# Kernel optimization log

Measured on AMD Instinct MI355X. Metric: run time of the kernel, lower is better.

The kernel has to match this reference:

```python
import jax, jax.numpy as jnp
import numpy as np

N = 100_000   # nodes
E = 1_600_000 # edges
D = 128       # input feature dim
H = 128       # hidden dim


def _lin_params(key, fan_in, fan_out):
    # torch nn.Linear default init: U(-1/sqrt(fan_in), 1/sqrt(fan_in))
    kw, kb = jax.random.split(key)
    s = 1.0 / np.sqrt(fan_in)
    W = jax.random.uniform(kw, (fan_in, fan_out), jnp.float32, -s, s)
    b = jax.random.uniform(kb, (fan_out,), jnp.float32, -s, s)
    return W, b


def setup_inputs() -> dict:
    key = jax.random.key(0)
    ks = jax.random.split(key, 9)
    x = jax.random.normal(ks[0], (N, D), jnp.float32)
    edge_index = jax.random.randint(ks[1], (2, E), 0, N)
    W1, b1 = _lin_params(ks[2], D, H)   # GCN layer 1
    W2, b2 = _lin_params(ks[3], H, H)   # GCN layer 2
    W3, b3 = _lin_params(ks[4], H, H)   # GCN layer 3
    sW1, sb1 = _lin_params(ks[5], 2 * H, 2 * H)  # scorer MLP
    sW2, sb2 = _lin_params(ks[6], 2 * H, H)
    sW3, sb3 = _lin_params(ks[7], H, 1)
    return {"x": x, "edge_index": edge_index,
            "W1": W1, "b1": b1, "W2": W2, "b2": b2, "W3": W3, "b3": b3,
            "sW1": sW1, "sb1": sb1, "sW2": sW2, "sb2": sb2, "sW3": sW3, "sb3": sb3}


def gcn_conv(h, src, tgt, W, b, n_nodes):
    # PyG GCNConv: add self-loops, D^{-1/2}(A+I)D^{-1/2} X W + b
    h = h @ W  # [N, out]
    deg = jax.ops.segment_sum(jnp.ones(src.shape[0], h.dtype), tgt,
                              num_segments=n_nodes) + 1.0  # +1 for self-loop
    dis = jax.lax.rsqrt(deg)                               # deg>=1 so finite
    coef = dis[src] * dis[tgt]                             # [E]
    agg = jax.ops.segment_sum(h[src] * coef[:, None], tgt, num_segments=n_nodes)
    agg = agg + h * (dis * dis)[:, None]                   # self-loop messages
    return agg + b


def reference(x, edge_index, W1, b1, W2, b2, W3, b3, sW1, sb1, sW2, sb2, sW3, sb3):
    src, tgt = edge_index[0], edge_index[1]
    n = x.shape[0]
    h = x
    for W, b in ((W1, b1), (W2, b2), (W3, b3)):
        h = jax.nn.relu(gcn_conv(h, src, tgt, W, b, n))
    node_embs = jnp.nan_to_num(h, nan=0.0)
    # edge scorer: gather src/tgt embeddings, concat, 3-layer MLP
    edge_feat = jnp.concatenate([node_embs[src], node_embs[tgt]], axis=1)  # [E, 2H]
    z = jax.nn.relu(edge_feat @ sW1 + sb1)
    z = jax.nn.relu(z @ sW2 + sb2)
    score = (z @ sW3 + sb3)[:, 0]  # [E]
    score = jnp.clip(score, -1e6, 1e6)
    score = jnp.nan_to_num(score, nan=0.0, posinf=1e6, neginf=-1e6)
    return score, node_embs
```

## Files before the change

kernel.cpp:

```cpp
#include <hip/hip_runtime.h>
#include <hip/hip_bf16.h>


#define SCORER_G 4

typedef __attribute__((ext_vector_type(8))) short bf16x8;
typedef __attribute__((ext_vector_type(4))) float f32x4;

__device__ __forceinline__ unsigned short f2bf(float x) {
  unsigned u = __float_as_uint(x);
  return (unsigned short)((u + 0x7FFFu + ((u >> 16) & 1u)) >> 16);
}
__device__ __forceinline__ float bf2f(unsigned short b) {
  return __uint_as_float(((unsigned)b) << 16);
}


__global__ __launch_bounds__(256) void zero_i32(int* __restrict__ p, int n) {
  int i = blockIdx.x * 256 + threadIdx.x;
  if (i < n) p[i] = 0;
}

__global__ __launch_bounds__(256) void deg_count(const int* __restrict__ tgt,
                                                 int* __restrict__ deg, int E) {
  int e = blockIdx.x * 256 + threadIdx.x;
  if (e < E) atomicAdd(&deg[tgt[e]], 1);
}

__global__ __launch_bounds__(256) void scan1(const int* __restrict__ deg,
                                             int* __restrict__ rowptr,
                                             int* __restrict__ bsum, int N) {
  __shared__ int s[256];
  int tid = threadIdx.x;
  int i = blockIdx.x * 256 + tid;
  int v = (i < N) ? deg[i] : 0;
  s[tid] = v;
  __syncthreads();
  for (int off = 1; off < 256; off <<= 1) {
    int t = (tid >= off) ? s[tid - off] : 0;
    __syncthreads();
    s[tid] += t;
    __syncthreads();
  }
  if (i < N) rowptr[i + 1] = s[tid];
  if (tid == 255) bsum[blockIdx.x] = s[255];
}

__global__ __launch_bounds__(512) void scan2(int* __restrict__ bsum, int nb) {
  __shared__ int s[512];
  int tid = threadIdx.x;
  int v = (tid < nb) ? bsum[tid] : 0;
  s[tid] = v;
  __syncthreads();
  for (int off = 1; off < 512; off <<= 1) {
    int t = (tid >= off) ? s[tid - off] : 0;
    __syncthreads();
    s[tid] += t;
    __syncthreads();
  }
  if (tid < nb) bsum[tid] = s[tid] - v;
}

__global__ __launch_bounds__(256) void scan3(int* __restrict__ rowptr,
                                             int* __restrict__ cursor,
                                             const int* __restrict__ bsum,
                                             float* __restrict__ dis, int N) {
  int i = blockIdx.x * 256 + threadIdx.x;
  if (i >= N) return;
  int incl = rowptr[i + 1] + bsum[blockIdx.x];
  rowptr[i + 1] = incl;
  int d = cursor[i];
  cursor[i] = incl - d;
  dis[i] = rsqrtf((float)d + 1.0f);
  if (i == 0) rowptr[0] = 0;
}

__global__ __launch_bounds__(256) void fill_k(const int* __restrict__ tgt,
                                              int* __restrict__ cursor,
                                              int* __restrict__ csr_eid, int E) {
  int e = blockIdx.x * 256 + threadIdx.x;
  if (e >= E) return;
  int pos = atomicAdd(&cursor[tgt[e]], 1);
  csr_eid[pos] = e;
}

__global__ __launch_bounds__(256) void wsplit_k(const float* __restrict__ sW2,
                                                unsigned short* __restrict__ Wth,
                                                unsigned short* __restrict__ Wtl) {
  int id = blockIdx.x * 256 + threadIdx.x;
  if (id >= 128 * 256) return;
  int n = id >> 8, k = id & 255;
  float v = sW2[k * 128 + n];
  unsigned short h = f2bf(v);
  Wth[id] = h;
  Wtl[id] = f2bf(v - bf2f(h));
}

__global__ __launch_bounds__(256) void gemm_k(const float* __restrict__ A,
                                              const float* __restrict__ W,
                                              float* __restrict__ out,
                                              int nRows, int nout) {
  __shared__ float As[64][36];
  __shared__ float Ws[32][128];
  const int tid  = threadIdx.x;
  const int row0 = blockIdx.x * 64;
  const int col0 = blockIdx.y * 128;
  const bool full = (row0 + 64 <= nRows);
  const int ty = tid >> 5, tx = tid & 31;
  const int r0 = ty * 8, c0 = tx * 4;
  float acc[8][4] = {};
  for (int kt = 0; kt < 128; kt += 32) {
    if (full) {
#pragma unroll
      for (int j = 0; j < 2; ++j) {
        int chunk = tid + j * 256;
        int r = chunk >> 3, c4 = (chunk & 7) * 4;
        *(float4*)(&As[r][c4]) =
            *(const float4*)(A + (size_t)(row0 + r) * 128 + kt + c4);
      }
    } else {
#pragma unroll
      for (int j = 0; j < 2; ++j) {
        int chunk = tid + j * 256;
        int r = chunk >> 3, c4 = (chunk & 7) * 4;
        float4 v = make_float4(0.f, 0.f, 0.f, 0.f);
        int gr = row0 + r;
        if (gr < nRows) v = *(const float4*)(A + (size_t)gr * 128 + kt + c4);
        *(float4*)(&As[r][c4]) = v;
      }
    }
#pragma unroll
    for (int j = 0; j < 4; ++j) {
      int chunk = tid + j * 256;
      int wr = chunk >> 5, wc4 = (chunk & 31) * 4;
      *(float4*)(&Ws[wr][wc4]) =
          *(const float4*)(W + (size_t)(kt + wr) * nout + col0 + wc4);
    }
    __syncthreads();
#pragma unroll
    for (int kk = 0; kk < 8; ++kk) {
      const float4 wv0 = *(const float4*)(&Ws[kk * 4 + 0][c0]);
      const float4 wv1 = *(const float4*)(&Ws[kk * 4 + 1][c0]);
      const float4 wv2 = *(const float4*)(&Ws[kk * 4 + 2][c0]);
      const float4 wv3 = *(const float4*)(&Ws[kk * 4 + 3][c0]);
#pragma unroll
      for (int i = 0; i < 8; ++i) {
        const float4 av = *(const float4*)(&As[r0 + i][kk * 4]);
        acc[i][0] += av.x * wv0.x + av.y * wv1.x + av.z * wv2.x + av.w * wv3.x;
        acc[i][1] += av.x * wv0.y + av.y * wv1.y + av.z * wv2.y + av.w * wv3.y;
        acc[i][2] += av.x * wv0.z + av.y * wv1.z + av.z * wv2.z + av.w * wv3.z;
        acc[i][3] += av.x * wv0.w + av.y * wv1.w + av.z * wv2.w + av.w * wv3.w;
      }
    }
    __syncthreads();
  }
#pragma unroll
  for (int i = 0; i < 8; ++i) {
    int gr = row0 + r0 + i;
    if (gr < nRows) {
      float4 v = make_float4(acc[i][0], acc[i][1], acc[i][2], acc[i][3]);
      *(float4*)(out + (size_t)gr * nout + col0 + c0) = v;
    }
  }
}

__global__ __launch_bounds__(256) void agg_k(const int* __restrict__ rowptr,
                                             const int* __restrict__ csr_eid,
                                             const int* __restrict__ src0,
                                             const float* __restrict__ dis,
                                             const float* __restrict__ hw,
                                             const float* __restrict__ bias,
                                             float* __restrict__ out, int N) {
  int i = (blockIdx.x * 256 + threadIdx.x) >> 6;
  if (i >= N) return;
  int l = threadIdx.x & 63;
  const float di = dis[i];
  const float2 bb = *(const float2*)(bias + l * 2);
  float2 acc = *(const float2*)(hw + (size_t)i * 128 + l * 2);
  float sc = di * di;
  acc.x *= sc; acc.y *= sc;
  int e = rowptr[i], e1 = rowptr[i + 1];
  for (; e + 1 < e1; e += 2) {
    int eA = csr_eid[e], eB = csr_eid[e + 1];
    int sA = src0[eA], sB = src0[eB];
    float cA = dis[sA] * di, cB = dis[sB] * di;
    const float2 vA = *(const float2*)(hw + (size_t)sA * 128 + l * 2);
    const float2 vB = *(const float2*)(hw + (size_t)sB * 128 + l * 2);
    acc.x += vA.x * cA + vB.x * cB;
    acc.y += vA.y * cA + vB.y * cB;
  }
  if (e < e1) {
    int eA = csr_eid[e];
    int sA = src0[eA];
    float cA = dis[sA] * di;
    const float2 vA = *(const float2*)(hw + (size_t)sA * 128 + l * 2);
    acc.x += vA.x * cA;
    acc.y += vA.y * cA;
  }
  acc.x = fmaxf(acc.x + bb.x, 0.f);
  acc.y = fmaxf(acc.y + bb.y, 0.f);
  *(float2*)(out + (size_t)i * 128 + l * 2) = acc;
}

__global__ __launch_bounds__(512, 4) void scorer_k(
    const float* __restrict__ Amat, const float* __restrict__ Bmat,
    const int* __restrict__ csr_eid, const int* __restrict__ src0,
    const int* __restrict__ tgt0, const float* __restrict__ sb1,
    const unsigned short* __restrict__ Wth,
    const unsigned short* __restrict__ Wtl,
    const float* __restrict__ sb2, const float* __restrict__ sW3,
    const float* __restrict__ sb3, float* __restrict__ score, int E) {
  __shared__ unsigned short z1h[64][256];
  __shared__ unsigned short z1l[64][256];
  __shared__ float psum[2][64];
  const int tid  = threadIdx.x;
  const int lane = tid & 63;
  const int wv   = tid >> 6;
  const int mb   = wv & 3;
  const int half = wv >> 2;
  const int l15  = lane & 15;
  const int l4   = lane >> 4;
  const float4 bb  = *(const float4*)(sb1 + lane * 4);
  const float sb3s = sb3[0];
  float sb2q[4], w3q[4];
#pragma unroll
  for (int q = 0; q < 4; ++q) {
    int col = (half * 4 + q) * 16 + l15;
    sb2q[q] = sb2[col];
    w3q[q]  = sW3[col];
  }
  char* z1h_b = (char*)&z1h[0][0];
  char* z1l_b = (char*)&z1l[0][0];

  for (int g = 0; g < SCORER_G; ++g) {
    const int e0 = (blockIdx.x * SCORER_G + g) * 64;
    if (e0 >= E) break;

#pragma unroll
    for (int j = 0; j < 8; ++j) {
      int row = wv * 8 + j;
      int e = e0 + row;
      if (e >= E) e = E - 1;
      int eid = csr_eid[e];
      int s = src0[eid], t = tgt0[eid];
      float4 a = *(const float4*)(Amat + (size_t)s * 256 + lane * 4);
      float4 b = *(const float4*)(Bmat + (size_t)t * 256 + lane * 4);
      float z0 = fmaxf(a.x + b.x + bb.x, 0.f);
      float z1v = fmaxf(a.y + b.y + bb.y, 0.f);
      float z2v = fmaxf(a.z + b.z + bb.z, 0.f);
      float z3v = fmaxf(a.w + b.w + bb.w, 0.f);
      ushort4 hp, lp;
      hp.x = f2bf(z0);  lp.x = f2bf(z0 - bf2f(hp.x));
      hp.y = f2bf(z1v); lp.y = f2bf(z1v - bf2f(hp.y));
      hp.z = f2bf(z2v); lp.z = f2bf(z2v - bf2f(hp.z));
      hp.w = f2bf(z3v); lp.w = f2bf(z3v - bf2f(hp.w));
      int bofs = (row * 512 + lane * 8) ^ ((row & 7) << 4);
      *(ushort4*)(z1h_b + bofs) = hp;
      *(ushort4*)(z1l_b + bofs) = lp;
    }
    __syncthreads();

    f32x4 acc0 = {0.f, 0.f, 0.f, 0.f};
    f32x4 acc1 = acc0, acc2 = acc0, acc3 = acc0;
    const int arow = mb * 16 + l15;
    const int aswz = (arow & 7) << 4;
#pragma unroll
    for (int kts = 0; kts < 8; ++kts) {
      int abofs = (arow * 512 + kts * 64 + l4 * 16) ^ aswz;
      bf16x8 ah = *(const bf16x8*)(z1h_b + abofs);
      bf16x8 al = *(const bf16x8*)(z1l_b + abofs);
      const int kof = kts * 32 + l4 * 8;
#define BQ(q)                                                                 \
      {                                                                       \
        int n = (half * 4 + (q)) * 16 + l15;                                  \
        bf16x8 bh = *(const bf16x8*)(Wth + n * 256 + kof);                    \
        bf16x8 bl = *(const bf16x8*)(Wtl + n * 256 + kof);                    \
        acc##q = __builtin_amdgcn_mfma_f32_16x16x32_bf16(al, bh, acc##q, 0, 0, 0); \
        acc##q = __builtin_amdgcn_mfma_f32_16x16x32_bf16(ah, bl, acc##q, 0, 0, 0); \
        acc##q = __builtin_amdgcn_mfma_f32_16x16x32_bf16(ah, bh, acc##q, 0, 0, 0); \
      }
      BQ(0) BQ(1) BQ(2) BQ(3)
#undef BQ
    }

    float t0 = 0.f, t1 = 0.f, t2 = 0.f, t3 = 0.f;
#define EQ(q)                                                   \
    t0 += fmaxf(acc##q[0] + sb2q[q], 0.f) * w3q[q];             \
    t1 += fmaxf(acc##q[1] + sb2q[q], 0.f) * w3q[q];             \
    t2 += fmaxf(acc##q[2] + sb2q[q], 0.f) * w3q[q];             \
    t3 += fmaxf(acc##q[3] + sb2q[q], 0.f) * w3q[q];
    EQ(0) EQ(1) EQ(2) EQ(3)
#undef EQ
#pragma unroll
    for (int m = 8; m >= 1; m >>= 1) {
      t0 += __shfl_xor(t0, m, 64);
      t1 += __shfl_xor(t1, m, 64);
      t2 += __shfl_xor(t2, m, 64);
      t3 += __shfl_xor(t3, m, 64);
    }
    if (l15 == 0) {
      int rb = mb * 16 + l4 * 4;
      psum[half][rb + 0] = t0;
      psum[half][rb + 1] = t1;
      psum[half][rb + 2] = t2;
      psum[half][rb + 3] = t3;
    }
    __syncthreads();
    if (tid < 64) {
      float v = psum[0][tid] + psum[1][tid] + sb3s;
      v = fminf(fmaxf(v, -1e6f), 1e6f);
      if (v != v) v = 0.f;
      int e = e0 + tid;
      if (e < E) score[csr_eid[e]] = v;
    }
    __syncthreads();
  }
}


extern "C" void kernel_launch(void* const* d_in, const int* in_sizes, int n_in,
                              void* d_out, int out_size, void* d_ws, size_t ws_size,
                              hipStream_t stream) {
  const float* x   = (const float*)d_in[0];
  const int*   ei  = (const int*)d_in[1];
  const float* W1  = (const float*)d_in[2];
  const float* b1  = (const float*)d_in[3];
  const float* W2  = (const float*)d_in[4];
  const float* b2  = (const float*)d_in[5];
  const float* W3  = (const float*)d_in[6];
  const float* b3  = (const float*)d_in[7];
  const float* sW1 = (const float*)d_in[8];
  const float* sb1 = (const float*)d_in[9];
  const float* sW2 = (const float*)d_in[10];
  const float* sb2 = (const float*)d_in[11];
  const float* sW3 = (const float*)d_in[12];
  const float* sb3 = (const float*)d_in[13];

  const int N = in_sizes[0] / 128;
  const int E = in_sizes[1] / 2;
  const int* src0 = ei;
  const int* tgt0 = ei + E;

  float* out_score = (float*)d_out;
  float* out_emb   = out_score + E;

  float* ws = (float*)d_ws;
  float* dis     = ws;
  int*   rowptr  = (int*)(dis + N);
  int*   csr_eid = rowptr + (N + 4);
  float* Abuf    = (float*)(csr_eid + E);
  float* Bbuf    = Abuf + (size_t)N * 256;
  unsigned short* Wth = (unsigned short*)(Bbuf + (size_t)N * 256);
  unsigned short* Wtl = Wth + 128 * 256;
  int*   cursor  = (int*)Abuf;
  int*   bsum    = cursor + N;
  float* hw      = Abuf;

  const dim3 blk(256);
  const int gN  = (N + 255) / 256;
  const int gE  = (E + 255) / 256;
  const int gRows = (N + 63) / 64;
  const int gAgg  = (N * 64 + 255) / 256;
  const int nT64  = (E + 63) / 64;
  const int gScore = (nT64 + SCORER_G - 1) / SCORER_G;

  zero_i32<<<gN, blk, 0, stream>>>(cursor, N);
  deg_count<<<gE, blk, 0, stream>>>(tgt0, cursor, E);
  scan1<<<gN, blk, 0, stream>>>(cursor, rowptr, bsum, N);
  scan2<<<1, 512, 0, stream>>>(bsum, gN);
  scan3<<<gN, blk, 0, stream>>>(rowptr, cursor, bsum, dis, N);
  fill_k<<<gE, blk, 0, stream>>>(tgt0, cursor, csr_eid, E);

  wsplit_k<<<128, blk, 0, stream>>>(sW2, Wth, Wtl);

  gemm_k<<<dim3(gRows, 1), blk, 0, stream>>>(x, W1, hw, N, 128);
  agg_k<<<gAgg, blk, 0, stream>>>(rowptr, csr_eid, src0, dis, hw, b1, out_emb, N);
  gemm_k<<<dim3(gRows, 1), blk, 0, stream>>>(out_emb, W2, hw, N, 128);
  agg_k<<<gAgg, blk, 0, stream>>>(rowptr, csr_eid, src0, dis, hw, b2, out_emb, N);
  gemm_k<<<dim3(gRows, 1), blk, 0, stream>>>(out_emb, W3, hw, N, 128);
  agg_k<<<gAgg, blk, 0, stream>>>(rowptr, csr_eid, src0, dis, hw, b3, out_emb, N);

  gemm_k<<<dim3(gRows, 2), blk, 0, stream>>>(out_emb, sW1, Abuf, N, 256);
  gemm_k<<<dim3(gRows, 2), blk, 0, stream>>>(out_emb, sW1 + 128 * 256, Bbuf, N, 256);

  scorer_k<<<gScore, dim3(512), 0, stream>>>(Abuf, Bbuf, csr_eid, src0, tgt0,
                                             sb1, Wth, Wtl, sb2, sW3, sb3,
                                             out_score, E);
}
```

Measured before the change: 3.087 ms.

## Keep scorer W2 tiles in registers and split waves by output column

```diff
diff --git a/kernel.cpp b/kernel.cpp
--- a/kernel.cpp
+++ b/kernel.cpp
@@ -212,102 +212,116 @@
     const float* __restrict__ sb3, float* __restrict__ score, int E) {
   __shared__ unsigned short z1h[64][256];
   __shared__ unsigned short z1l[64][256];
-  __shared__ float psum[2][64];
+  __shared__ float psum[8][64];
   const int tid  = threadIdx.x;
   const int lane = tid & 63;
   const int wv   = tid >> 6;
-  const int mb   = wv & 3;
-  const int half = wv >> 2;
   const int l15  = lane & 15;
   const int l4   = lane >> 4;
   const float4 bb  = *(const float4*)(sb1 + lane * 4);
   const float sb3s = sb3[0];
-  float sb2q[4], w3q[4];
-#pragma unroll
-  for (int q = 0; q < 4; ++q) {
-    int col = (half * 4 + q) * 16 + l15;
-    sb2q[q] = sb2[col];
-    w3q[q]  = sW3[col];
-  }
+  const int col   = wv * 16 + l15;
+  const float sb2c = sb2[col];
+  const float w3c  = sW3[col];
   char* z1h_b = (char*)&z1h[0][0];
   char* z1l_b = (char*)&z1l[0][0];
+
+  bf16x8 bh[8], bl[8];
+#pragma unroll
+  for (int kts = 0; kts < 8; ++kts) {
+    size_t wofs = (size_t)col * 256 + kts * 32 + l4 * 8;
+    bh[kts] = *(const bf16x8*)(Wth + wofs);
+    bl[kts] = *(const bf16x8*)(Wtl + wofs);
+  }
 
   for (int g = 0; g < SCORER_G; ++g) {
     const int e0 = (blockIdx.x * SCORER_G + g) * 64;
     if (e0 >= E) break;
 
 #pragma unroll
-    for (int j = 0; j < 8; ++j) {
-      int row = wv * 8 + j;
-      int e = e0 + row;
-      if (e >= E) e = E - 1;
-      int eid = csr_eid[e];
-      int s = src0[eid], t = tgt0[eid];
-      float4 a = *(const float4*)(Amat + (size_t)s * 256 + lane * 4);
-      float4 b = *(const float4*)(Bmat + (size_t)t * 256 + lane * 4);
-      float z0 = fmaxf(a.x + b.x + bb.x, 0.f);
-      float z1v = fmaxf(a.y + b.y + bb.y, 0.f);
-      float z2v = fmaxf(a.z + b.z + bb.z, 0.f);
-      float z3v = fmaxf(a.w + b.w + bb.w, 0.f);
+    for (int jj = 0; jj < 8; jj += 2) {
+      int rowA = wv * 8 + jj, rowB = rowA + 1;
+      int eA = e0 + rowA; if (eA >= E) eA = E - 1;
+      int eB = e0 + rowB; if (eB >= E) eB = E - 1;
+      int eidA = csr_eid[eA], eidB = csr_eid[eB];
+      int sA = src0[eidA], tA = tgt0[eidA];
+      int sB = src0[eidB], tB = tgt0[eidB];
+      float4 aA = *(const float4*)(Amat + (size_t)sA * 256 + lane * 4);
+      float4 bA = *(const float4*)(Bmat + (size_t)tA * 256 + lane * 4);
+      float4 aB = *(const float4*)(Amat + (size_t)sB * 256 + lane * 4);
+      float4 bB = *(const float4*)(Bmat + (size_t)tB * 256 + lane * 4);
+      float zA0 = fmaxf(aA.x + bA.x + bb.x, 0.f);
+      float zA1 = fmaxf(aA.y + bA.y + bb.y, 0.f);
+      float zA2 = fmaxf(aA.z + bA.z + bb.z, 0.f);
+      float zA3 = fmaxf(aA.w + bA.w + bb.w, 0.f);
+      float zB0 = fmaxf(aB.x + bB.x + bb.x, 0.f);
+      float zB1 = fmaxf(aB.y + bB.y + bb.y, 0.f);
+      float zB2 = fmaxf(aB.z + bB.z + bb.z, 0.f);
+      float zB3 = fmaxf(aB.w + bB.w + bb.w, 0.f);
       ushort4 hp, lp;
-      hp.x = f2bf(z0);  lp.x = f2bf(z0 - bf2f(hp.x));
-      hp.y = f2bf(z1v); lp.y = f2bf(z1v - bf2f(hp.y));
-      hp.z = f2bf(z2v); lp.z = f2bf(z2v - bf2f(hp.z));
-      hp.w = f2bf(z3v); lp.w = f2bf(z3v - bf2f(hp.w));
-      int bofs = (row * 512 + lane * 8) ^ ((row & 7) << 4);
-      *(ushort4*)(z1h_b + bofs) = hp;
-      *(ushort4*)(z1l_b + bofs) = lp;
+      hp.x = f2bf(zA0); lp.x = f2bf(zA0 - bf2f(hp.x));
+      hp.y = f2bf(zA1); lp.y = f2bf(zA1 - bf2f(hp.y));
+      hp.z = f2bf(zA2); lp.z = f2bf(zA2 - bf2f(hp.z));
+      hp.w = f2bf(zA3); lp.w = f2bf(zA3 - bf2f(hp.w));
+      int bofsA = (rowA * 512 + lane * 8) ^ ((rowA & 7) << 4);
+      *(ushort4*)(z1h_b + bofsA) = hp;
+      *(ushort4*)(z1l_b + bofsA) = lp;
+      hp.x = f2bf(zB0); lp.x = f2bf(zB0 - bf2f(hp.x));
+      hp.y = f2bf(zB1); lp.y = f2bf(zB1 - bf2f(hp.y));
+      hp.z = f2bf(zB2); lp.z = f2bf(zB2 - bf2f(hp.z));
+      hp.w = f2bf(zB3); lp.w = f2bf(zB3 - bf2f(hp.w));
+      int bofsB = (rowB * 512 + lane * 8) ^ ((rowB & 7) << 4);
+      *(ushort4*)(z1h_b + bofsB) = hp;
+      *(ushort4*)(z1l_b + bofsB) = lp;
     }
     __syncthreads();
 
     f32x4 acc0 = {0.f, 0.f, 0.f, 0.f};
     f32x4 acc1 = acc0, acc2 = acc0, acc3 = acc0;
-    const int arow = mb * 16 + l15;
-    const int aswz = (arow & 7) << 4;
 #pragma unroll
     for (int kts = 0; kts < 8; ++kts) {
-      int abofs = (arow * 512 + kts * 64 + l4 * 16) ^ aswz;
-      bf16x8 ah = *(const bf16x8*)(z1h_b + abofs);
-      bf16x8 al = *(const bf16x8*)(z1l_b + abofs);
-      const int kof = kts * 32 + l4 * 8;
-#define BQ(q)                                                                 \
+#define RB(rb)                                                                \
       {                                                                       \
-        int n = (half * 4 + (q)) * 16 + l15;                                  \
-        bf16x8 bh = *(const bf16x8*)(Wth + n * 256 + kof);                    \
-        bf16x8 bl = *(const bf16x8*)(Wtl + n * 256 + kof);                    \
-        acc##q = __builtin_amdgcn_mfma_f32_16x16x32_bf16(al, bh, acc##q, 0, 0, 0); \
-        acc##q = __builtin_amdgcn_mfma_f32_16x16x32_bf16(ah, bl, acc##q, 0, 0, 0); \
-        acc##q = __builtin_amdgcn_mfma_f32_16x16x32_bf16(ah, bh, acc##q, 0, 0, 0); \
+        int arow = (rb) * 16 + l15;                                           \
+        int abofs = (arow * 512 + kts * 64 + l4 * 16) ^ ((arow & 7) << 4);    \
+        bf16x8 ah = *(const bf16x8*)(z1h_b + abofs);                          \
+        bf16x8 al = *(const bf16x8*)(z1l_b + abofs);                          \
+        acc##rb = __builtin_amdgcn_mfma_f32_16x16x32_bf16(al, bh[kts], acc##rb, 0, 0, 0); \
+        acc##rb = __builtin_amdgcn_mfma_f32_16x16x32_bf16(ah, bl[kts], acc##rb, 0, 0, 0); \
+        acc##rb = __builtin_amdgcn_mfma_f32_16x16x32_bf16(ah, bh[kts], acc##rb, 0, 0, 0); \
       }
-      BQ(0) BQ(1) BQ(2) BQ(3)
-#undef BQ
-    }
-
-    float t0 = 0.f, t1 = 0.f, t2 = 0.f, t3 = 0.f;
-#define EQ(q)                                                   \
-    t0 += fmaxf(acc##q[0] + sb2q[q], 0.f) * w3q[q];             \
-    t1 += fmaxf(acc##q[1] + sb2q[q], 0.f) * w3q[q];             \
-    t2 += fmaxf(acc##q[2] + sb2q[q], 0.f) * w3q[q];             \
-    t3 += fmaxf(acc##q[3] + sb2q[q], 0.f) * w3q[q];
-    EQ(0) EQ(1) EQ(2) EQ(3)
-#undef EQ
-#pragma unroll
-    for (int m = 8; m >= 1; m >>= 1) {
-      t0 += __shfl_xor(t0, m, 64);
-      t1 += __shfl_xor(t1, m, 64);
-      t2 += __shfl_xor(t2, m, 64);
-      t3 += __shfl_xor(t3, m, 64);
-    }
-    if (l15 == 0) {
-      int rb = mb * 16 + l4 * 4;
-      psum[half][rb + 0] = t0;
-      psum[half][rb + 1] = t1;
-      psum[half][rb + 2] = t2;
-      psum[half][rb + 3] = t3;
-    }
+      RB(0) RB(1) RB(2) RB(3)
+#undef RB
+    }
+
+#define EPI(rb)                                                               \
+    {                                                                         \
+      float t0 = fmaxf(acc##rb[0] + sb2c, 0.f) * w3c;                         \
+      float t1 = fmaxf(acc##rb[1] + sb2c, 0.f) * w3c;                         \
+      float t2 = fmaxf(acc##rb[2] + sb2c, 0.f) * w3c;                         \
+      float t3 = fmaxf(acc##rb[3] + sb2c, 0.f) * w3c;                         \
+      _Pragma("unroll")                                                       \
+      for (int m = 8; m >= 1; m >>= 1) {                                      \
+        t0 += __shfl_xor(t0, m, 64);                                          \
+        t1 += __shfl_xor(t1, m, 64);                                          \
+        t2 += __shfl_xor(t2, m, 64);                                          \
+        t3 += __shfl_xor(t3, m, 64);                                          \
+      }                                                                       \
+      if (l15 == 0) {                                                         \
+        int rbase = (rb) * 16 + l4 * 4;                                       \
+        psum[wv][rbase + 0] = t0;                                             \
+        psum[wv][rbase + 1] = t1;                                             \
+        psum[wv][rbase + 2] = t2;                                             \
+        psum[wv][rbase + 3] = t3;                                             \
+      }                                                                       \
+    }
+    EPI(0) EPI(1) EPI(2) EPI(3)
+#undef EPI
     __syncthreads();
     if (tid < 64) {
-      float v = psum[0][tid] + psum[1][tid] + sb3s;
+      float v = psum[0][tid] + psum[1][tid] + psum[2][tid] + psum[3][tid] +
+                psum[4][tid] + psum[5][tid] + psum[6][tid] + psum[7][tid] +
+                sb3s;
       v = fminf(fmaxf(v, -1e6f), 1e6f);
       if (v != v) v = 0.f;
       int e = e0 + tid;
```

Result: faster. 2.657 ms (-13.9%).
